# Performance work log

Hardware: AMD Instinct MI355X
Metric: run time of the kernel (lower is better)

The kernel has to match this reference:

```python
import jax, jax.numpy as jnp
import numpy as np
import math

T, NF, DF = 215, 36, 215      # timesteps, sensor nodes, GIN feature dim
D_PE, D_MODEL = 28, 64
BN_EPS = 1e-5


def _bn_eval(x, gamma, beta, mean, var):
    return (x - mean) * jax.lax.rsqrt(var + BN_EPS) * gamma + beta


def _gin(x, src_i, tgt_i, w1, b1, gamma, beta, mean, var, w2, b2):
    # GINConv (eps=0): nn(x + sum_{j->i} x_j); scatter-add over edge list
    agg = jax.ops.segment_sum(x[src_i], tgt_i, num_segments=x.shape[0])
    h = x + agg
    h = jax.nn.relu(_bn_eval(h @ w1 + b1, gamma, beta, mean, var))
    return jax.nn.relu(h @ w2 + b2)


def _edge_index(adj):
    # adj.triu() + adj.triu(1).T -> symmetric; nonzero (dense w.p. 1 -> 1296)
    adj_sym = jnp.triu(adj) + jnp.triu(adj, 1).T
    rows, cols = jnp.nonzero(adj_sym, size=NF * NF, fill_value=0)
    # direct edges (rows->cols targets per PyG flow) then inverse edges appended
    src_i = jnp.concatenate([rows, cols])
    tgt_i = jnp.concatenate([cols, rows])
    return src_i, tgt_i


def _pos_encode(times):
    # PositionalEncodingTF with d_pe=28 -> 14 timescales, base max_len=215
    ts = jnp.asarray(float(T) ** np.linspace(0.0, 1.0, D_PE // 2), dtype=times.dtype)
    scaled = times[..., None] / ts                      # [T,B,14]
    return jnp.concatenate([jnp.sin(scaled), jnp.cos(scaled)], axis=-1)  # [T,B,28]


def setup_inputs() -> dict:
    key = jax.random.key(0)
    ks = jax.random.split(key, 24)
    B = 4096
    f32 = jnp.float32
    rn = lambda k, s, sc=1.0: jax.random.normal(k, s, dtype=f32) * sc
    inp = {
        'src': rn(ks[0], (T, B, NF)),
        'static': rn(ks[1], (B, 9)),
        'times': jax.random.uniform(ks[2], (T, B), dtype=f32) * float(T),
        'lengths': jax.random.randint(ks[3], (B,), 1, T, dtype=jnp.int32),
        'adj': rn(ks[4], (NF, NF), math.sqrt(6.0 / (NF + NF))),
        'enc_w': rn(ks[5], (NF, NF), 0.05), 'enc_b': jnp.zeros((NF,), f32),
        'emb_w': rn(ks[6], (9, D_MODEL), 0.05), 'emb_b': jnp.zeros((D_MODEL,), f32),
        'mlp_w1': rn(ks[7], (D_MODEL, D_MODEL), 0.1), 'mlp_b1': jnp.zeros((D_MODEL,), f32),
        'mlp_w2': rn(ks[8], (D_MODEL, 2), 0.1), 'mlp_b2': jnp.zeros((2,), f32),
    }
    for i, pfx in enumerate(['g1', 'g2']):
        kk = jax.random.split(ks[9 + i], 4)
        inp[pfx + '_w1'] = rn(kk[0], (DF, DF), 0.05)
        inp[pfx + '_b1'] = jnp.zeros((DF,), f32)
        inp[pfx + '_gamma'] = 1.0 + rn(kk[1], (DF,), 0.1)
        inp[pfx + '_beta'] = rn(kk[2], (DF,), 0.1)
        inp[pfx + '_mean'] = jnp.zeros((DF,), f32)
        inp[pfx + '_var'] = jnp.ones((DF,), f32)
        inp[pfx + '_w2'] = rn(kk[3], (DF, DF), 0.05)
        inp[pfx + '_b2'] = jnp.zeros((DF,), f32)
    return inp


def reference(src, static, times, lengths, adj, enc_w, enc_b, emb_w, emb_b,
              g1_w1, g1_b1, g1_gamma, g1_beta, g1_mean, g1_var, g1_w2, g1_b2,
              g2_w1, g2_b1, g2_gamma, g2_beta, g2_mean, g2_var, g2_w2, g2_b2,
              mlp_w1, mlp_b1, mlp_w2, mlp_b2):
    maxlen, B = src.shape[0], src.shape[1]
    # encoder + scale (dropout is identity in eval)
    h = (src @ enc_w + enc_b) * math.sqrt(float(D_MODEL))          # [T,B,36]
    pe = _pos_encode(times)                                        # [T,B,28]
    emb = static @ emb_w + emb_b                                   # [B,64]
    src_i, tgt_i = _edge_index(adj)
    # GIN over flattened node rows; edges only touch nodes 0..35 (as in source)
    x = h.transpose(1, 2, 0).reshape(-1, DF)                       # [B*36,215]
    x = _gin(x, src_i, tgt_i, g1_w1, g1_b1, g1_gamma, g1_beta, g1_mean, g1_var, g1_w2, g1_b2)
    x = _gin(x, src_i, tgt_i, g2_w1, g2_b1, g2_gamma, g2_beta, g2_mean, g2_var, g2_w2, g2_b2)
    out = x.reshape(-1, NF, DF).transpose(2, 0, 1)                 # [215,B,36]
    out = jnp.concatenate([pe, out], axis=2)                       # [215,B,64]
    full = jnp.concatenate([emb[None], out], axis=0)               # [216,B,64]
    # mask rows past lengths+1, mean-aggregate over time
    mask = jnp.arange(maxlen + 1)[None, :] >= (lengths[:, None] + 1)  # [B,216]
    w = (1.0 - mask.T[..., None].astype(full.dtype))               # [216,B,1]
    agg = jnp.sum(full * w, axis=0) / (lengths[:, None] + 1).astype(full.dtype)
    return jax.nn.relu(agg @ mlp_w1 + mlp_b1) @ mlp_w2 + mlp_b2    # [B,2]
```

## Files before the change

### kernel.cpp

```cpp
#include <hip/hip_runtime.h>
#include <math.h>

#define T_LEN 215
#define BATCH 4096
#define NFEAT 36
#define DF 215
#define KP 224
#define NROWS (BATCH*NFEAT)
#define WP 256
#define WROWS 224
#define WELEMS (WROWS*WP)

typedef __bf16 v8bf __attribute__((ext_vector_type(8)));
typedef float f32x16 __attribute__((ext_vector_type(16)));

static __device__ __forceinline__ float bf2f(ushort u) {
    return __uint_as_float(((uint)u) << 16);
}
static __device__ __forceinline__ ushort f2bf(float f) {
    uint x = __float_as_uint(f);
    return (ushort)((x + 0x7FFFu + ((x >> 16) & 1u)) >> 16);
}

__global__ __launch_bounds__(256) void wprep_kernel(
    const float* __restrict__ w1a, const float* __restrict__ w2a,
    const float* __restrict__ w1b, const float* __restrict__ w2b,
    ushort* __restrict__ wt)
{
    const float* src = (blockIdx.z == 0) ? w1a : (blockIdx.z == 1) ? w2a
                     : (blockIdx.z == 2) ? w1b : w2b;
    ushort* dst = wt + (size_t)blockIdx.z * WELEMS;
    __shared__ float tile[32][33];
    int k0 = blockIdx.x * 32, h0 = blockIdx.y * 32;
    int j = threadIdx.x & 31, i0 = threadIdx.x >> 5;
    for (int i = i0; i < 32; i += 8) {
        int k = k0 + i, h = h0 + j;
        tile[i][j] = (k < DF && h < DF) ? src[(size_t)k * DF + h] : 0.f;
    }
    __syncthreads();
    for (int i = i0; i < 32; i += 8) {
        int h = h0 + i;
        int ks = (k0 + j) ^ ((h & 7) << 3);
        dst[(size_t)h * WP + ks] = f2bf(tile[j][i]);
    }
    if (blockIdx.x == 6) {
        for (int i = i0; i < 32; i += 8) {
            int h = h0 + i;
            int ks = (224 + j) ^ ((h & 7) << 3);
            dst[(size_t)h * WP + ks] = 0;
        }
    }
}

__global__ __launch_bounds__(256) void enc_kernel(const float* __restrict__ src,
    const float* __restrict__ enc_w, const float* __restrict__ enc_b,
    ushort* __restrict__ X0)
{
    __shared__ float sw[NFEAT*NFEAT];
    __shared__ float sb[NFEAT];
    __shared__ float st[64][NFEAT+1];
    int tid = threadIdx.x;
    int b   = blockIdx.x;
    int t0  = blockIdx.y * 64;
    int nt  = min(64, T_LEN - t0);

    for (int i = tid; i < NFEAT*NFEAT; i += 256) sw[i] = enc_w[i];
    if (tid < NFEAT) sb[tid] = enc_b[tid];
    for (int i = tid; i < nt*NFEAT; i += 256) {
        int ti = i / NFEAT, m = i - ti*NFEAT;
        st[ti][m] = src[((size_t)(t0+ti)*BATCH + b)*NFEAT + m];
    }
    __syncthreads();

    for (int o = tid; o < NFEAT*nt; o += 256) {
        int n = o / nt, ti = o - n*nt;
        float acc = sb[n];
        #pragma unroll
        for (int m = 0; m < NFEAT; ++m) acc = fmaf(st[ti][m], sw[m*NFEAT+n], acc);
        X0[(size_t)(b*NFEAT + n)*KP + t0 + ti] = f2bf(acc * 8.0f);
    }
    if (t0 + 64 > T_LEN) {
        for (int i = tid; i < NFEAT*(KP - T_LEN); i += 256) {
            int n = i / (KP - T_LEN), o = i % (KP - T_LEN);
            X0[(size_t)(b*NFEAT + n)*KP + T_LEN + o] = 0;
        }
    }
}

__global__ void colsum_kernel(const ushort* __restrict__ X, float* __restrict__ S)
{
    int t = threadIdx.x;
    if (t < KP) {
        float s = 0.f;
        #pragma unroll
        for (int n = 0; n < NFEAT; ++n) s += bf2f(X[n*KP + t]);
        S[t] = 2.0f * s;
    }
}

__global__ __launch_bounds__(512, 1) void gin_mfma_kernel(
    ushort* __restrict__ X, const float* __restrict__ S2,
    const ushort* __restrict__ Wt1, const ushort* __restrict__ Wt2,
    const float* __restrict__ B1v, const float* __restrict__ Gm,
    const float* __restrict__ Bt,  const float* __restrict__ Mn,
    const float* __restrict__ Vr,  const float* __restrict__ B2v)
{
    __shared__ ushort wlds[WELEMS];
    __shared__ float bnsc[224], bnsh[224], b2s[224];

    int tid  = threadIdx.x;
    int lane = tid & 63, wv = tid >> 6;
    int ml   = lane & 31, half = lane >> 5;
    int row  = blockIdx.x * 256 + wv * 32 + ml;

    if (tid < 224) {
        if (tid < DF) {
            float sc = Gm[tid] * rsqrtf(Vr[tid] + 1e-5f);
            bnsc[tid] = sc;
            bnsh[tid] = fmaf(B1v[tid] - Mn[tid], sc, Bt[tid]);
            b2s[tid]  = B2v[tid];
        } else { bnsc[tid] = 0.f; bnsh[tid] = 0.f; b2s[tid] = 0.f; }
    }
    {
        const uint4* s = (const uint4*)Wt1;
        uint4* d = (uint4*)wlds;
        for (int i = tid; i < WELEMS/8; i += 512) d[i] = s[i];
    }

    ushort* xr = X + (size_t)row * KP;
    bool agg = row < NFEAT;
    uint4 B1[14];
    #pragma unroll
    for (int kb = 0; kb < 14; ++kb) {
        uint4 r = *(const uint4*)(xr + kb*16 + half*8);
        if (agg) {
            int k0 = kb*16 + half*8;
            uint w0 = r.x, w1 = r.y, w2 = r.z, w3 = r.w;
            float a0 = bf2f((ushort)(w0 & 0xffff)) + S2[k0+0];
            float a1 = bf2f((ushort)(w0 >> 16))    + S2[k0+1];
            float a2 = bf2f((ushort)(w1 & 0xffff)) + S2[k0+2];
            float a3 = bf2f((ushort)(w1 >> 16))    + S2[k0+3];
            float a4 = bf2f((ushort)(w2 & 0xffff)) + S2[k0+4];
            float a5 = bf2f((ushort)(w2 >> 16))    + S2[k0+5];
            float a6 = bf2f((ushort)(w3 & 0xffff)) + S2[k0+6];
            float a7 = bf2f((ushort)(w3 >> 16))    + S2[k0+7];
            r.x = ((uint)f2bf(a1) << 16) | f2bf(a0);
            r.y = ((uint)f2bf(a3) << 16) | f2bf(a2);
            r.z = ((uint)f2bf(a5) << 16) | f2bf(a4);
            r.w = ((uint)f2bf(a7) << 16) | f2bf(a6);
        }
        B1[kb] = r;
    }
    __syncthreads();

    uint4 B2[14];
    #pragma unroll
    for (int ht = 0; ht < 7; ++ht) {
        f32x16 acc;
        #pragma unroll
        for (int r = 0; r < 16; ++r) acc[r] = 0.f;
        #pragma unroll
        for (int kb = 0; kb < 14; ++kb) {
            int rrow = ht*32 + ml;
            int by = rrow*512 + ((kb*32 + half*16) ^ ((rrow & 7) << 4));
            uint4 a = *(const uint4*)((const char*)wlds + by);
            acc = __builtin_amdgcn_mfma_f32_32x32x16_bf16(
                      __builtin_bit_cast(v8bf, a),
                      __builtin_bit_cast(v8bf, B1[kb]), acc, 0, 0, 0);
        }
        int hb = ht*32;
        uint d[8];
        #pragma unroll
        for (int p = 0; p < 8; ++p) {
            int r0 = 2*p;
            int h0i = hb + (r0 & 3) + 8*(r0 >> 2) + 4*half;
            float v0 = fmaxf(fmaf(acc[r0],   bnsc[h0i],   bnsh[h0i]),   0.f);
            float v1 = fmaxf(fmaf(acc[r0+1], bnsc[h0i+1], bnsh[h0i+1]), 0.f);
            d[p] = ((uint)f2bf(v1) << 16) | f2bf(v0);
        }
        uint ea = __shfl_xor(half ? d[0] : d[2], 32);
        uint eb = __shfl_xor(half ? d[1] : d[3], 32);
        uint ec = __shfl_xor(half ? d[4] : d[6], 32);
        uint ed = __shfl_xor(half ? d[5] : d[7], 32);
        B2[2*ht]   = half ? make_uint4(ea, eb, d[2], d[3])
                          : make_uint4(d[0], d[1], ea, eb);
        B2[2*ht+1] = half ? make_uint4(ec, ed, d[6], d[7])
                          : make_uint4(d[4], d[5], ec, ed);
    }
    __syncthreads();
    {
        const uint4* s = (const uint4*)Wt2;
        uint4* d = (uint4*)wlds;
        for (int i = tid; i < WELEMS/8; i += 512) d[i] = s[i];
    }
    __syncthreads();

    #pragma unroll
    for (int nt = 0; nt < 7; ++nt) {
        f32x16 acc;
        #pragma unroll
        for (int r = 0; r < 16; ++r) acc[r] = 0.f;
        #pragma unroll
        for (int kb = 0; kb < 14; ++kb) {
            int rrow = nt*32 + ml;
            int by = rrow*512 + ((kb*32 + half*16) ^ ((rrow & 7) << 4));
            uint4 a = *(const uint4*)((const char*)wlds + by);
            acc = __builtin_amdgcn_mfma_f32_32x32x16_bf16(
                      __builtin_bit_cast(v8bf, a),
                      __builtin_bit_cast(v8bf, B2[kb]), acc, 0, 0, 0);
        }
        int nb = nt*32;
        #pragma unroll
        for (int g = 0; g < 4; ++g) {
            int r0 = 4*g;
            int n0 = nb + 8*g + 4*half;
            float v0 = fmaxf(acc[r0]   + b2s[n0],   0.f);
            float v1 = fmaxf(acc[r0+1] + b2s[n0+1], 0.f);
            float v2 = fmaxf(acc[r0+2] + b2s[n0+2], 0.f);
            float v3 = fmaxf(acc[r0+3] + b2s[n0+3], 0.f);
            uint lo = ((uint)f2bf(v1) << 16) | f2bf(v0);
            uint hi = ((uint)f2bf(v3) << 16) | f2bf(v2);
            if (n0 + 3 < DF) {
                *(uint2*)(xr + n0) = make_uint2(lo, hi);
            } else {
                if (n0     < DF) xr[n0]     = (ushort)(lo & 0xffff);
                if (n0 + 1 < DF) xr[n0 + 1] = (ushort)(lo >> 16);
                if (n0 + 2 < DF) xr[n0 + 2] = (ushort)(hi & 0xffff);
            }
        }
    }
}

__device__ inline float wave_sum(float v) {
    #pragma unroll
    for (int off = 32; off > 0; off >>= 1) v += __shfl_down(v, off);
    return v;
}

__global__ __launch_bounds__(256) void final_kernel(const ushort* __restrict__ Y2,
    const float* __restrict__ times, const int* __restrict__ lengths,
    const float* __restrict__ stat, const float* __restrict__ emb_w,
    const float* __restrict__ emb_b, const float* __restrict__ w1,
    const float* __restrict__ b1, const float* __restrict__ w2,
    const float* __restrict__ b2, float* __restrict__ out)
{
    int b = blockIdx.x, tid = threadIdx.x;
    int lane = tid & 63, w = tid >> 6;
    int L = lengths[b];
    __shared__ float aggs[64];
    __shared__ float red[4][28];
    __shared__ float hsh[64];

    #pragma unroll
    for (int q = 0; q < 9; ++q) {
        int n = w*9 + q;
        const ushort* row = Y2 + (size_t)(b*NFEAT + n)*KP;
        float s = 0.f;
        for (int t = lane; t < L; t += 64) s += bf2f(row[t]);
        s = wave_sum(s);
        if (lane == 0) aggs[28 + n] = s;
    }

    float psin[14], pcos[14];
    #pragma unroll
    for (int k = 0; k < 14; ++k) { psin[k] = 0.f; pcos[k] = 0.f; }
    if (tid < L) {
        float x = times[(size_t)tid*BATCH + b];
        #pragma unroll
        for (int k = 0; k < 14; ++k) {
            float arg = x * exp2f(-0.59601508f * (float)k);
            float s, c;
            sincosf(arg, &s, &c);
            psin[k] = s; pcos[k] = c;
        }
    }
    #pragma unroll
    for (int k = 0; k < 14; ++k) {
        float v = wave_sum(psin[k]);
        if (lane == 0) red[w][k] = v;
        v = wave_sum(pcos[k]);
        if (lane == 0) red[w][14 + k] = v;
    }
    __syncthreads();
    if (tid < 28) aggs[tid] = red[0][tid] + red[1][tid] + red[2][tid] + red[3][tid];
    __syncthreads();

    if (tid < 64) {
        float e = emb_b[tid];
        #pragma unroll
        for (int m = 0; m < 9; ++m) e = fmaf(stat[b*9 + m], emb_w[m*64 + tid], e);
        aggs[tid] = (aggs[tid] + e) / (float)(L + 1);
    }
    __syncthreads();

    if (tid < 64) {
        float a = b1[tid];
        #pragma unroll
        for (int f = 0; f < 64; ++f) a = fmaf(aggs[f], w1[f*64 + tid], a);
        hsh[tid] = fmaxf(a, 0.f);
    }
    __syncthreads();
    if (tid < 2) {
        float a = b2[tid];
        #pragma unroll
        for (int j = 0; j < 64; ++j) a = fmaf(hsh[j], w2[j*2 + tid], a);
        out[b*2 + tid] = a;
    }
}

extern "C" void kernel_launch(void* const* d_in, const int* in_sizes, int n_in,
                              void* d_out, int out_size, void* d_ws, size_t ws_size,
                              hipStream_t stream)
{
    const float* src     = (const float*)d_in[0];
    const float* stat    = (const float*)d_in[1];
    const float* times   = (const float*)d_in[2];
    const int*   lengths = (const int*)  d_in[3];
    const float* enc_w   = (const float*)d_in[5];
    const float* enc_b   = (const float*)d_in[6];
    const float* emb_w   = (const float*)d_in[7];
    const float* emb_b   = (const float*)d_in[8];
    const float* mlp_w1  = (const float*)d_in[9];
    const float* mlp_b1  = (const float*)d_in[10];
    const float* mlp_w2  = (const float*)d_in[11];
    const float* mlp_b2  = (const float*)d_in[12];
    const float* g1_w1   = (const float*)d_in[13];
    const float* g1_b1   = (const float*)d_in[14];
    const float* g1_gm   = (const float*)d_in[15];
    const float* g1_bt   = (const float*)d_in[16];
    const float* g1_mn   = (const float*)d_in[17];
    const float* g1_vr   = (const float*)d_in[18];
    const float* g1_w2   = (const float*)d_in[19];
    const float* g1_b2   = (const float*)d_in[20];
    const float* g2_w1   = (const float*)d_in[21];
    const float* g2_b1   = (const float*)d_in[22];
    const float* g2_gm   = (const float*)d_in[23];
    const float* g2_bt   = (const float*)d_in[24];
    const float* g2_mn   = (const float*)d_in[25];
    const float* g2_vr   = (const float*)d_in[26];
    const float* g2_w2   = (const float*)d_in[27];
    const float* g2_b2   = (const float*)d_in[28];

    ushort* X0 = (ushort*)d_ws;
    ushort* Wt = X0 + (size_t)NROWS * KP;
    float*  S  = (float*)(Wt + 4 * (size_t)WELEMS);

    wprep_kernel<<<dim3(7, 7, 4), 256, 0, stream>>>(g1_w1, g1_w2, g2_w1, g2_w2, Wt);
    enc_kernel<<<dim3(BATCH, 4), 256, 0, stream>>>(src, enc_w, enc_b, X0);

    colsum_kernel<<<1, 256, 0, stream>>>(X0, S);
    gin_mfma_kernel<<<NROWS/256, 512, 0, stream>>>(X0, S, Wt, Wt + WELEMS,
        g1_b1, g1_gm, g1_bt, g1_mn, g1_vr, g1_b2);

    colsum_kernel<<<1, 256, 0, stream>>>(X0, S);
    gin_mfma_kernel<<<NROWS/256, 512, 0, stream>>>(X0, S, Wt + 2*WELEMS, Wt + 3*WELEMS,
        g2_b1, g2_gm, g2_bt, g2_mn, g2_vr, g2_b2);

    final_kernel<<<BATCH, 256, 0, stream>>>(X0, times, lengths, stat, emb_w, emb_b,
                                            mlp_w1, mlp_b1, mlp_w2, mlp_b2,
                                            (float*)d_out);
}
```

Before: 576.2 us.

## Restructure encoder to one block per batch and fuse first column-sum

The encoder kernel now processes all timesteps of a batch element in one block. Each thread computes all 36 outputs for one timestep in registers, reading weights from global or constant cache instead of shared memory. Source rows are loaded with float4 vector loads. Block 0 also produces the column sums for the first GIN layer, which removes a separate colsum launch. Costs: heavier register pressure per thread, and the column sum now uses unrounded fp32 values rather than the bf16-rounded ones.

```diff
diff --git a/kernel.cpp b/kernel.cpp
--- a/kernel.cpp
+++ b/kernel.cpp
@@ -54,35 +54,51 @@
 
 __global__ __launch_bounds__(256) void enc_kernel(const float* __restrict__ src,
     const float* __restrict__ enc_w, const float* __restrict__ enc_b,
-    ushort* __restrict__ X0)
-{
-    __shared__ float sw[NFEAT*NFEAT];
-    __shared__ float sb[NFEAT];
-    __shared__ float st[64][NFEAT+1];
+    ushort* __restrict__ X0, float* __restrict__ S)
+{
+    __shared__ float st[T_LEN * NFEAT];
     int tid = threadIdx.x;
     int b   = blockIdx.x;
-    int t0  = blockIdx.y * 64;
-    int nt  = min(64, T_LEN - t0);
-
-    for (int i = tid; i < NFEAT*NFEAT; i += 256) sw[i] = enc_w[i];
-    if (tid < NFEAT) sb[tid] = enc_b[tid];
-    for (int i = tid; i < nt*NFEAT; i += 256) {
-        int ti = i / NFEAT, m = i - ti*NFEAT;
-        st[ti][m] = src[((size_t)(t0+ti)*BATCH + b)*NFEAT + m];
-    }
-    __syncthreads();
-
-    for (int o = tid; o < NFEAT*nt; o += 256) {
-        int n = o / nt, ti = o - n*nt;
-        float acc = sb[n];
-        #pragma unroll
-        for (int m = 0; m < NFEAT; ++m) acc = fmaf(st[ti][m], sw[m*NFEAT+n], acc);
-        X0[(size_t)(b*NFEAT + n)*KP + t0 + ti] = f2bf(acc * 8.0f);
-    }
-    if (t0 + 64 > T_LEN) {
-        for (int i = tid; i < NFEAT*(KP - T_LEN); i += 256) {
-            int n = i / (KP - T_LEN), o = i % (KP - T_LEN);
-            X0[(size_t)(b*NFEAT + n)*KP + T_LEN + o] = 0;
+
+    for (int i = tid; i < T_LEN * 9; i += 256) {
+        int t = i / 9, q = i - t * 9;
+        *(float4*)&st[t*NFEAT + q*4] =
+            *(const float4*)(src + ((size_t)t*BATCH + b)*NFEAT + q*4);
+    }
+    __syncthreads();
+
+    int t = tid;
+    if (t < KP) {
+        float acc[NFEAT];
+        if (t < T_LEN) {
+            float x[NFEAT];
+            #pragma unroll
+            for (int q = 0; q < 9; ++q)
+                *(float4*)&x[q*4] = *(const float4*)&st[t*NFEAT + q*4];
+            #pragma unroll
+            for (int n = 0; n < NFEAT; ++n) acc[n] = enc_b[n];
+            #pragma unroll 4
+            for (int m = 0; m < NFEAT; ++m) {
+                float xm = x[m];
+                #pragma unroll
+                for (int n = 0; n < NFEAT; ++n)
+                    acc[n] = fmaf(xm, enc_w[m*NFEAT + n], acc[n]);
+            }
+            #pragma unroll
+            for (int n = 0; n < NFEAT; ++n) acc[n] *= 8.0f;
+        } else {
+            #pragma unroll
+            for (int n = 0; n < NFEAT; ++n) acc[n] = 0.f;
+        }
+        size_t base = (size_t)b * NFEAT * KP;
+        #pragma unroll
+        for (int n = 0; n < NFEAT; ++n)
+            X0[base + (size_t)n*KP + t] = f2bf(acc[n]);
+        if (b == 0) {
+            float s = 0.f;
+            #pragma unroll
+            for (int n = 0; n < NFEAT; ++n) s += acc[n];
+            S[t] = 2.0f * s;
         }
     }
 }
@@ -346,9 +362,8 @@
     float*  S  = (float*)(Wt + 4 * (size_t)WELEMS);
 
     wprep_kernel<<<dim3(7, 7, 4), 256, 0, stream>>>(g1_w1, g1_w2, g2_w1, g2_w2, Wt);
-    enc_kernel<<<dim3(BATCH, 4), 256, 0, stream>>>(src, enc_w, enc_b, X0);
-
-    colsum_kernel<<<1, 256, 0, stream>>>(X0, S);
+    enc_kernel<<<BATCH, 256, 0, stream>>>(src, enc_w, enc_b, X0, S);
+
     gin_mfma_kernel<<<NROWS/256, 512, 0, stream>>>(X0, S, Wt, Wt + WELEMS,
         g1_b1, g1_gm, g1_bt, g1_mn, g1_vr, g1_b2);
 
```

Result: faster. 524.2 us (-9.0%).
